# Performance work log

Hardware: AMD Instinct MI355X
Metric: run time of the kernel (lower is better)

## Reference

```python
import jax, jax.numpy as jnp
import numpy as np

H = 16      # num_heads
D = 1024    # input_dim
F = 4096    # feed_forward_hidden_size
B, S = 8, 4096
EPS = 1e-6


def _ln(x, g, b):
    mu = jnp.mean(x, axis=-1, keepdims=True)
    var = jnp.mean(jnp.square(x - mu), axis=-1, keepdims=True)
    return (x - mu) * jax.lax.rsqrt(var + EPS) * g + b


def _attn(Q, K, V):
    # per-head attention; original scales by sqrt(input_dim), NOT sqrt(head_dim)
    b, sq, d = Q.shape
    sk = K.shape[1]
    dh = d // H
    Qh = Q.reshape(b, sq, H, dh)
    Kh = K.reshape(b, sk, H, dh)
    Vh = V.reshape(b, sk, H, dh)
    scores = jnp.einsum('bqhd,bkhd->bhqk', Qh, Kh) / jnp.sqrt(jnp.float32(d))
    w = jax.nn.softmax(scores, axis=-1)
    return jnp.einsum('bhqk,bkhd->bqhd', w, Vh).reshape(b, sq, d)


def setup_inputs() -> dict:
    key = jax.random.key(0)
    ks = jax.random.split(key, 10)
    sc = 0.02
    np.random.seed(42)
    decode_input = jnp.asarray(np.random.random([B, 1, D]).astype(np.float32))
    return {
        'key': jax.random.normal(ks[0], (B, S, D), jnp.float32),
        'value': jax.random.normal(ks[1], (B, S, D), jnp.float32),
        'decode_input': decode_input,
        'Wq': jax.random.normal(ks[2], (D, D), jnp.float32) * sc,
        'bq': jnp.zeros((D,), jnp.float32),
        'Wk': jax.random.normal(ks[3], (D, D), jnp.float32) * sc,
        'bk': jnp.zeros((D,), jnp.float32),
        'Wv': jax.random.normal(ks[4], (D, D), jnp.float32) * sc,
        'bv': jnp.zeros((D,), jnp.float32),
        'Wo': jax.random.normal(ks[5], (D, D), jnp.float32) * sc,
        'bo': jnp.zeros((D,), jnp.float32),
        'W1': jax.random.normal(ks[6], (D, F), jnp.float32) * sc,
        'b1': jnp.zeros((F,), jnp.float32),
        'W2': jax.random.normal(ks[7], (F, D), jnp.float32) * sc,
        'b2': jnp.zeros((D,), jnp.float32),
        'ln2_g': jnp.ones((D,), jnp.float32),
        'ln2_b': jnp.zeros((D,), jnp.float32),
        'lnf_g': jnp.ones((D,), jnp.float32),
        'lnf_b': jnp.zeros((D,), jnp.float32),
    }


def reference(key, value, decode_input, Wq, bq, Wk, bk, Wv, bv, Wo, bo,
              W1, b1, W2, b2, ln2_g, ln2_b, lnf_g, lnf_b):
    # K/V projections shared by both attention calls (original reuses mha_1)
    K = key @ Wk + bk            # [B,S,D]
    V = value @ Wv + bv          # [B,S,D]

    # mha_1: self-attention of decode_input would use its own K/V, but here
    # q=k=v=decode_input for the first call
    Q1 = decode_input @ Wq + bq
    K1 = decode_input @ Wk + bk
    V1 = decode_input @ Wv + bv
    mha1_out = _attn(Q1, K1, V1) @ Wo + bo   # [B,1,D]
    # note: layer_norm_mha_1 output is computed in original but never used

    # second call (original buggily calls mha_1 again): q=mha1_out (un-normed)
    Q2 = mha1_out @ Wq + bq
    mha2_out = _attn(Q2, K, V) @ Wo + bo     # [B,1,D]
    x = _ln(mha2_out + decode_input, ln2_g, ln2_b)

    ff = jax.nn.relu(x @ W1 + b1) @ W2 + b2
    return _ln(ff + x, lnf_g, lnf_b)
```

## Files before the change

kernel.cpp:

```cpp
#include <hip/hip_runtime.h>
#include <hip/hip_bf16.h>

#define NB 8
#define NS 4096
#define ND 1024
#define NH 16
#define NF 4096

typedef __attribute__((ext_vector_type(8))) short s16x8;
typedef __attribute__((ext_vector_type(4))) float f32x4;

__device__ __forceinline__ short f2bfs(float x) {
    __hip_bfloat16 h = __float2bfloat16(x);
    return *reinterpret_cast<short*>(&h);
}

__device__ __forceinline__ s16x8 pack8v(f32x4 a, f32x4 b) {
    s16x8 r;
    r[0]=f2bfs(a[0]); r[1]=f2bfs(a[1]); r[2]=f2bfs(a[2]); r[3]=f2bfs(a[3]);
    r[4]=f2bfs(b[0]); r[5]=f2bfs(b[1]); r[6]=f2bfs(b[2]); r[7]=f2bfs(b[3]);
    return r;
}


template<int KC>
__global__ void __launch_bounds__(256) mvV_k(const float* __restrict__ x,
        const float* __restrict__ W, int K, int Cout, float* __restrict__ Pout)
{
    __shared__ float xs[KC * 8];
    int tid = threadIdx.x;
    int c = blockIdx.x * 256 + tid;
    int k0 = blockIdx.y * KC;
    for (int i = tid; i < KC * 8; i += 256) {
        int k = i >> 3, b = i & 7;
        xs[i] = x[(size_t)b * K + k0 + k];
    }
    __syncthreads();
    const float* Wp = W + (size_t)k0 * Cout + c;
    float acc[8] = {0,0,0,0,0,0,0,0};
    #pragma unroll 16
    for (int k = 0; k < KC; ++k) {
        float wv = Wp[(size_t)k * Cout];
        float4 x0 = *(const float4*)&xs[k * 8];
        float4 x1 = *(const float4*)&xs[k * 8 + 4];
        acc[0] += x0.x * wv; acc[1] += x0.y * wv; acc[2] += x0.z * wv; acc[3] += x0.w * wv;
        acc[4] += x1.x * wv; acc[5] += x1.y * wv; acc[6] += x1.z * wv; acc[7] += x1.w * wv;
    }
    float* op = Pout + ((size_t)blockIdx.y * 8) * Cout + c;
    #pragma unroll
    for (int b = 0; b < 8; ++b) op[(size_t)b * Cout] = acc[b];
}

template<int KC, int NP, int RELU>
__global__ void __launch_bounds__(256) mvP_k(const float* __restrict__ P,
        const float* __restrict__ bias, const float* __restrict__ W,
        int K, int Cout, float* __restrict__ Pout)
{
    __shared__ float xs[KC * 8];
    int tid = threadIdx.x;
    int c = blockIdx.x * 256 + tid;
    int k0 = blockIdx.y * KC;
    for (int i = tid; i < KC * 8; i += 256) {
        int b = i / KC, k = i % KC;
        float t = bias[k0 + k];
        #pragma unroll 8
        for (int p = 0; p < NP; ++p) t += P[((size_t)(p * 8 + b)) * K + k0 + k];
        if (RELU) t = fmaxf(t, 0.f);
        xs[k * 8 + b] = t;
    }
    __syncthreads();
    const float* Wp = W + (size_t)k0 * Cout + c;
    float acc[8] = {0,0,0,0,0,0,0,0};
    #pragma unroll 16
    for (int k = 0; k < KC; ++k) {
        float wv = Wp[(size_t)k * Cout];
        float4 x0 = *(const float4*)&xs[k * 8];
        float4 x1 = *(const float4*)&xs[k * 8 + 4];
        acc[0] += x0.x * wv; acc[1] += x0.y * wv; acc[2] += x0.z * wv; acc[3] += x0.w * wv;
        acc[4] += x1.x * wv; acc[5] += x1.y * wv; acc[6] += x1.z * wv; acc[7] += x1.w * wv;
    }
    float* op = Pout + ((size_t)blockIdx.y * 8) * Cout + c;
    #pragma unroll
    for (int b = 0; b < 8; ++b) op[(size_t)b * Cout] = acc[b];
}

__global__ void __launch_bounds__(256) u_k(const float* __restrict__ P,
        const float* __restrict__ bq, const float* __restrict__ Wk,
        unsigned short* __restrict__ u16)
{
    int bh = blockIdx.x;
    int b = bh >> 4, h = bh & 15;
    int lane = threadIdx.x & 63, wv = threadIdx.x >> 6;
    int cc = h * 64 + lane;
    float q = bq[cc];
    #pragma unroll 8
    for (int p = 0; p < 64; ++p) q += P[((size_t)(p * 8 + b)) * 1024 + cc];
    int dbase = blockIdx.y * 256;
    #pragma unroll 4
    for (int d = dbase + wv; d < dbase + 256; d += 4) {
        float v = Wk[(size_t)d * 1024 + cc] * q;
        for (int off = 32; off; off >>= 1) v += __shfl_down(v, off);
        if (lane == 0) u16[(size_t)bh * 1024 + d] = (unsigned short)f2bfs(v);
    }
}

__global__ void __launch_bounds__(256) lnp_k(const float* __restrict__ P, int np,
        const float* __restrict__ bias, const float* __restrict__ add,
        const float* __restrict__ g, const float* __restrict__ be,
        float* __restrict__ out)
{
    int b = blockIdx.x, tid = threadIdx.x;
    __shared__ float sd[4];
    int c = tid * 4;
    f32x4 t = *(const f32x4*)&bias[c];
    t += *(const f32x4*)&add[(size_t)b * 1024 + c];
    #pragma unroll 8
    for (int p = 0; p < np; ++p)
        t += *(const f32x4*)&P[((size_t)(p * 8 + b)) * 1024 + c];
    float loc = t[0] + t[1] + t[2] + t[3];
    for (int off = 32; off; off >>= 1) loc += __shfl_down(loc, off);
    if ((tid & 63) == 0) sd[tid >> 6] = loc;
    __syncthreads();
    float mu = (sd[0] + sd[1] + sd[2] + sd[3]) * (1.f / 1024.f);
    __syncthreads();
    f32x4 d = t - mu;
    float v = d[0]*d[0] + d[1]*d[1] + d[2]*d[2] + d[3]*d[3];
    for (int off = 32; off; off >>= 1) v += __shfl_down(v, off);
    if ((tid & 63) == 0) sd[tid >> 6] = v;
    __syncthreads();
    float var = (sd[0] + sd[1] + sd[2] + sd[3]) * (1.f / 1024.f);
    float rs = rsqrtf(var + 1e-6f);
    f32x4 gg = *(const f32x4*)&g[c];
    f32x4 bb = *(const f32x4*)&be[c];
    f32x4 o = d * rs * gg + bb;
    *(f32x4*)&out[(size_t)b * 1024 + c] = o;
}

__global__ void __launch_bounds__(256) attn_k(const float* __restrict__ key,
        const float* __restrict__ value, const unsigned short* __restrict__ u16,
        float* __restrict__ plp, float* __restrict__ dnm)
{
    __shared__ __align__(16) unsigned short ul[16][1032];
    __shared__ __align__(16) float plT[64][16];
    int b = blockIdx.x, ch = blockIdx.y, tid = threadIdx.x;
    int s0 = ch * 64;

    const uint4* src = (const uint4*)(u16 + (size_t)b * NH * 1024);
    for (int v = tid; v < 2048; v += 256) {
        int h = v >> 7, col = (v & 127) * 8;
        *(uint4*)&ul[h][col] = src[v];
    }
    __syncthreads();

    {
        int lane = tid & 63, wv = tid >> 6;
        int r = lane & 15, g = lane >> 4;
        const float* kp0 = key + ((size_t)(b * NS + s0 + wv * 16 + r)) * ND + g * 8;
        f32x4 acc = {0.f, 0.f, 0.f, 0.f};
        #pragma unroll 4
        for (int k = 0; k < 1024; k += 32) {
            f32x4 x0 = __builtin_nontemporal_load((const f32x4*)(kp0 + k));
            f32x4 x1 = __builtin_nontemporal_load((const f32x4*)(kp0 + k + 4));
            s16x8 a = *(const s16x8*)&ul[r][k + g * 8];
            acc = __builtin_amdgcn_mfma_f32_16x16x32_bf16(a, pack8v(x0, x1), acc, 0, 0, 0);
        }
        const float scl = 1.f / 32.f;
        f32x4 e;
        e[0] = __expf(acc[0] * scl); e[1] = __expf(acc[1] * scl);
        e[2] = __expf(acc[2] * scl); e[3] = __expf(acc[3] * scl);
        *(f32x4*)&plT[wv * 16 + r][g * 4] = e;
    }
    __syncthreads();

    if (tid < 16) {
        float s = 0.f;
        #pragma unroll 16
        for (int si = 0; si < 64; ++si) s += plT[si][tid];
        dnm[((size_t)(ch * 8 + b)) * 16 + tid] = s;
    }

    {
        const f32x4* vp = (const f32x4*)(value + ((size_t)(b * NS + s0)) * ND) + tid;
        f32x4 acc[16];
        #pragma unroll
        for (int h = 0; h < 16; ++h) acc[h] = (f32x4){0.f, 0.f, 0.f, 0.f};
        #pragma unroll 4
        for (int s = 0; s < 64; ++s) {
            f32x4 v = __builtin_nontemporal_load(&vp[(size_t)s * 256]);
            const f32x4* w = (const f32x4*)&plT[s][0];
            f32x4 w0 = w[0], w1 = w[1], w2 = w[2], w3 = w[3];
            acc[0]  += v * w0[0]; acc[1]  += v * w0[1]; acc[2]  += v * w0[2]; acc[3]  += v * w0[3];
            acc[4]  += v * w1[0]; acc[5]  += v * w1[1]; acc[6]  += v * w1[2]; acc[7]  += v * w1[3];
            acc[8]  += v * w2[0]; acc[9]  += v * w2[1]; acc[10] += v * w2[2]; acc[11] += v * w2[3];
            acc[12] += v * w3[0]; acc[13] += v * w3[1]; acc[14] += v * w3[2]; acc[15] += v * w3[3];
        }
        float* o = plp + ((size_t)((ch * 8 + b) * 16)) * 1024 + tid * 4;
        #pragma unroll
        for (int h = 0; h < 16; ++h) *(f32x4*)(o + (size_t)h * 1024) = acc[h];
    }
}

template<int KC, int NCH>
__global__ void __launch_bounds__(256) mvH_k(const float* __restrict__ plp,
        const float* __restrict__ dnm, const float* __restrict__ W,
        float* __restrict__ Pout)
{
    __shared__ float xs[4 * KC * 8];
    int tid = threadIdx.x, lane = tid & 63, wv = tid >> 6;
    int c = blockIdx.x * 256 + tid;
    int k0 = blockIdx.y * KC;
    int h = blockIdx.x * 4 + wv;
    float den = 0.f;
    if (lane < 8) {
        #pragma unroll 8
        for (int ch = 0; ch < NCH; ++ch)
            den += dnm[((size_t)(ch * 8 + lane)) * 16 + h];
    }
    float inv8 = (lane < 8) ? 1.f / den : 0.f;
    for (int i = lane; i < 8 * KC; i += 64) {
        int b = i / KC, k = i % KC;
        float t = 0.f;
        #pragma unroll 8
        for (int ch = 0; ch < NCH; ++ch)
            t += plp[((size_t)((ch * 8 + b) * 16 + h)) * 1024 + k0 + k];
        xs[wv * 8 * KC + k * 8 + b] = t * __shfl(inv8, b);
    }
    __syncthreads();
    const float* Wp = W + (size_t)k0 * 1024 + c;
    float acc[8] = {0,0,0,0,0,0,0,0};
    #pragma unroll 16
    for (int k = 0; k < KC; ++k) {
        float wvv = Wp[(size_t)k * 1024];
        float4 x0 = *(const float4*)&xs[wv * 8 * KC + k * 8];
        float4 x1 = *(const float4*)&xs[wv * 8 * KC + k * 8 + 4];
        acc[0] += x0.x * wvv; acc[1] += x0.y * wvv; acc[2] += x0.z * wvv; acc[3] += x0.w * wvv;
        acc[4] += x1.x * wvv; acc[5] += x1.y * wvv; acc[6] += x1.z * wvv; acc[7] += x1.w * wvv;
    }
    float* op = Pout + ((size_t)blockIdx.y * 8) * 1024 + c;
    #pragma unroll
    for (int b = 0; b < 8; ++b) op[(size_t)b * 1024] = acc[b];
}

extern "C" void kernel_launch(void* const* d_in, const int* in_sizes, int n_in,
                              void* d_out, int out_size, void* d_ws, size_t ws_size,
                              hipStream_t stream)
{
    const float* key   = (const float*)d_in[0];
    const float* value = (const float*)d_in[1];
    const float* dec   = (const float*)d_in[2];
    const float* Wq = (const float*)d_in[3];  const float* bq = (const float*)d_in[4];
    const float* Wk = (const float*)d_in[5];
    const float* Wv = (const float*)d_in[7];  const float* bv = (const float*)d_in[8];
    const float* Wo = (const float*)d_in[9];  const float* bo = (const float*)d_in[10];
    const float* W1 = (const float*)d_in[11]; const float* b1 = (const float*)d_in[12];
    const float* W2 = (const float*)d_in[13]; const float* b2 = (const float*)d_in[14];
    const float* g2 = (const float*)d_in[15]; const float* be2 = (const float*)d_in[16];
    const float* gf = (const float*)d_in[17]; const float* bef = (const float*)d_in[18];

    float* ws = (float*)d_ws;
    float* Pa   = ws;
    float* Pb   = Pa   + 524288;
    float* Pq   = Pb   + 524288;
    float* plp  = Pq   + 524288;
    float* dnm  = plp  + 8388608;
    float* Pd   = dnm  + 8192;
    float* Pe   = Pd   + 524288;
    float* Pff1 = Pe   + 524288;
    float* Pff2 = Pff1 + 524288;
    float* xbuf = Pff2 + 524288;
    unsigned short* u16 = (unsigned short*)(xbuf + 8192);
    float* outp = (float*)d_out;

    dim3 blk(256);

    mvV_k<16><<<dim3(4,64), blk, 0, stream>>>(dec, Wv, 1024, 1024, Pa);
    mvP_k<16,64,0><<<dim3(4,64), blk, 0, stream>>>(Pa, bv, Wo, 1024, 1024, Pb);
    mvP_k<16,64,0><<<dim3(4,64), blk, 0, stream>>>(Pb, bo, Wq, 1024, 1024, Pq);
    u_k<<<dim3(128,4), blk, 0, stream>>>(Pq, bq, Wk, u16);

    attn_k<<<dim3(8,64), blk, 0, stream>>>(key, value, u16, plp, dnm);

    mvH_k<16,64><<<dim3(4,64), blk, 0, stream>>>(plp, dnm, Wv, Pd);
    mvP_k<16,64,0><<<dim3(4,64), blk, 0, stream>>>(Pd, bv, Wo, 1024, 1024, Pe);
    lnp_k<<<dim3(8), blk, 0, stream>>>(Pe, 64, bo, dec, g2, be2, xbuf);

    mvV_k<64><<<dim3(16,16), blk, 0, stream>>>(xbuf, W1, 1024, 4096, Pff1);
    mvP_k<64,16,1><<<dim3(4,64), blk, 0, stream>>>(Pff1, b1, W2, 4096, 1024, Pff2);
    lnp_k<<<dim3(8), blk, 0, stream>>>(Pff2, 64, b2, xbuf, gf, bef, outp);

    (void)in_sizes; (void)n_in; (void)out_size; (void)ws_size;
}
```

Baseline: 161.0 us.

## Double attention block threads by splitting K-dim and sequence across waves

The attention kernel now runs 512 threads per block. The score MFMA loop is split across two waves per 16-row tile along the feature dimension, with the partial results reduced through shared memory. The PV accumulation is split into two 32-row sequence halves, each writing its own partial output. This raises latency hiding and memory parallelism for the key/value streams, but doubles the partial buffer, so the downstream mvH kernel now reduces 128 chunks instead of 64, adding extra traffic.

```diff
diff --git a/kernel.cpp b/kernel.cpp
--- a/kernel.cpp
+++ b/kernel.cpp
@@ -136,39 +136,51 @@
     *(f32x4*)&out[(size_t)b * 1024 + c] = o;
 }
 
-__global__ void __launch_bounds__(256) attn_k(const float* __restrict__ key,
+__global__ void __launch_bounds__(512) attn_k(const float* __restrict__ key,
         const float* __restrict__ value, const unsigned short* __restrict__ u16,
         float* __restrict__ plp, float* __restrict__ dnm)
 {
     __shared__ __align__(16) unsigned short ul[16][1032];
+    __shared__ __align__(16) float pacc[8][64][4];
     __shared__ __align__(16) float plT[64][16];
     int b = blockIdx.x, ch = blockIdx.y, tid = threadIdx.x;
     int s0 = ch * 64;
 
     const uint4* src = (const uint4*)(u16 + (size_t)b * NH * 1024);
-    for (int v = tid; v < 2048; v += 256) {
+    for (int v = tid; v < 2048; v += 512) {
         int h = v >> 7, col = (v & 127) * 8;
         *(uint4*)&ul[h][col] = src[v];
     }
     __syncthreads();
 
     {
-        int lane = tid & 63, wv = tid >> 6;
+        int lane = tid & 63, w = tid >> 6;
+        int t = w >> 1, kh = w & 1;
         int r = lane & 15, g = lane >> 4;
-        const float* kp0 = key + ((size_t)(b * NS + s0 + wv * 16 + r)) * ND + g * 8;
+        const float* kp0 = key + ((size_t)(b * NS + s0 + t * 16 + r)) * ND + kh * 512 + g * 8;
+        const unsigned short* ua = &ul[r][kh * 512 + g * 8];
         f32x4 acc = {0.f, 0.f, 0.f, 0.f};
         #pragma unroll 4
-        for (int k = 0; k < 1024; k += 32) {
+        for (int k = 0; k < 512; k += 32) {
             f32x4 x0 = __builtin_nontemporal_load((const f32x4*)(kp0 + k));
             f32x4 x1 = __builtin_nontemporal_load((const f32x4*)(kp0 + k + 4));
-            s16x8 a = *(const s16x8*)&ul[r][k + g * 8];
+            s16x8 a = *(const s16x8*)(ua + k);
             acc = __builtin_amdgcn_mfma_f32_16x16x32_bf16(a, pack8v(x0, x1), acc, 0, 0, 0);
         }
+        *(f32x4*)&pacc[w][lane][0] = acc;
+    }
+    __syncthreads();
+
+    if (tid < 256) {
+        int t = tid >> 6, lane = tid & 63;
+        int r = lane & 15, g = lane >> 4;
+        f32x4 acc = *(const f32x4*)&pacc[t * 2][lane][0];
+        acc += *(const f32x4*)&pacc[t * 2 + 1][lane][0];
         const float scl = 1.f / 32.f;
         f32x4 e;
         e[0] = __expf(acc[0] * scl); e[1] = __expf(acc[1] * scl);
         e[2] = __expf(acc[2] * scl); e[3] = __expf(acc[3] * scl);
-        *(f32x4*)&plT[wv * 16 + r][g * 4] = e;
+        *(f32x4*)&plT[t * 16 + r][g * 4] = e;
     }
     __syncthreads();
 
@@ -180,21 +192,22 @@
     }
 
     {
-        const f32x4* vp = (const f32x4*)(value + ((size_t)(b * NS + s0)) * ND) + tid;
+        int sg = tid >> 8, dt = tid & 255;
+        const f32x4* vp = (const f32x4*)(value + ((size_t)(b * NS + s0 + sg * 32)) * ND) + dt;
         f32x4 acc[16];
         #pragma unroll
         for (int h = 0; h < 16; ++h) acc[h] = (f32x4){0.f, 0.f, 0.f, 0.f};
         #pragma unroll 4
-        for (int s = 0; s < 64; ++s) {
+        for (int s = 0; s < 32; ++s) {
             f32x4 v = __builtin_nontemporal_load(&vp[(size_t)s * 256]);
-            const f32x4* w = (const f32x4*)&plT[s][0];
+            const f32x4* w = (const f32x4*)&plT[sg * 32 + s][0];
             f32x4 w0 = w[0], w1 = w[1], w2 = w[2], w3 = w[3];
             acc[0]  += v * w0[0]; acc[1]  += v * w0[1]; acc[2]  += v * w0[2]; acc[3]  += v * w0[3];
             acc[4]  += v * w1[0]; acc[5]  += v * w1[1]; acc[6]  += v * w1[2]; acc[7]  += v * w1[3];
             acc[8]  += v * w2[0]; acc[9]  += v * w2[1]; acc[10] += v * w2[2]; acc[11] += v * w2[3];
             acc[12] += v * w3[0]; acc[13] += v * w3[1]; acc[14] += v * w3[2]; acc[15] += v * w3[3];
         }
-        float* o = plp + ((size_t)((ch * 8 + b) * 16)) * 1024 + tid * 4;
+        float* o = plp + ((size_t)(((ch * 2 + sg) * 8 + b) * 16)) * 1024 + dt * 4;
         #pragma unroll
         for (int h = 0; h < 16; ++h) *(f32x4*)(o + (size_t)h * 1024) = acc[h];
     }
@@ -213,7 +226,7 @@
     float den = 0.f;
     if (lane < 8) {
         #pragma unroll 8
-        for (int ch = 0; ch < NCH; ++ch)
+        for (int ch = 0; ch < 64; ++ch)
             den += dnm[((size_t)(ch * 8 + lane)) * 16 + h];
     }
     float inv8 = (lane < 8) ? 1.f / den : 0.f;
@@ -262,7 +275,7 @@
     float* Pb   = Pa   + 524288;
     float* Pq   = Pb   + 524288;
     float* plp  = Pq   + 524288;
-    float* dnm  = plp  + 8388608;
+    float* dnm  = plp  + 16777216;
     float* Pd   = dnm  + 8192;
     float* Pe   = Pd   + 524288;
     float* Pff1 = Pe   + 524288;
@@ -278,9 +291,9 @@
     mvP_k<16,64,0><<<dim3(4,64), blk, 0, stream>>>(Pb, bo, Wq, 1024, 1024, Pq);
     u_k<<<dim3(128,4), blk, 0, stream>>>(Pq, bq, Wk, u16);
 
-    attn_k<<<dim3(8,64), blk, 0, stream>>>(key, value, u16, plp, dnm);
-
-    mvH_k<16,64><<<dim3(4,64), blk, 0, stream>>>(plp, dnm, Wv, Pd);
+    attn_k<<<dim3(8,64), dim3(512), 0, stream>>>(key, value, u16, plp, dnm);
+
+    mvH_k<16,128><<<dim3(4,64), blk, 0, stream>>>(plp, dnm, Wv, Pd);
     mvP_k<16,64,0><<<dim3(4,64), blk, 0, stream>>>(Pd, bv, Wo, 1024, 1024, Pe);
     lnp_k<<<dim3(8), blk, 0, stream>>>(Pe, 64, bo, dec, g2, be2, xbuf);
 
```

New measurement: 168.2 us. 4.4% more time.
